# Kernel optimization log

Measured on AMD Instinct MI355X. Metric: run time of the kernel, lower is better.

Reference implementation:

```python
import jax, jax.numpy as jnp
import numpy as np

T, B, H = 1024, 16, 1024
S = 2048


def setup_inputs() -> dict:
    key = jax.random.key(0)
    k1, k2, k3, k4 = jax.random.split(key, 4)
    output = jax.random.normal(k1, (T, B, H), dtype=jnp.float32)
    memory = jax.random.normal(k2, (S, B, H), dtype=jnp.float32)
    attn_mask = jnp.zeros((B, T, S), dtype=jnp.bool_)  # True = masked
    # linear_out: Linear(2H -> H); torch weight layout [out, in]
    W = jax.random.normal(k3, (H, 2 * H), dtype=jnp.float32) * (1.0 / np.sqrt(2 * H))
    b = jax.random.normal(k4, (H,), dtype=jnp.float32) * 0.01
    return {"output": output, "memory": memory, "attn_mask": attn_mask, "W": W, "b": b}


def reference(output, memory, attn_mask, W, b):
    # scores: (B, T, S) = output^T @ memory (unscaled dot product)
    attn = jnp.einsum('tbh,sbh->bts', output, memory)
    attn = jnp.where(attn_mask, -jnp.inf, attn)
    attn = jax.nn.softmax(attn, axis=2)
    # context: (T, B, H)
    context = jnp.einsum('bts,sbh->tbh', attn, memory)
    combined = jnp.concatenate([context, output], axis=2)  # (T, B, 2H)
    out = jnp.tanh(jnp.einsum('tbd,hd->tbh', combined, W) + b)
    return (out, attn)
```

## Files before the change

### kernel.cpp

```cpp
#include <hip/hip_runtime.h>
#include <hip/hip_bf16.h>
#include <math.h>

#define Tn 1024
#define Bn 16
#define Hn 1024
#define Sn 2048

typedef __attribute__((ext_vector_type(8))) short bf16x8;
typedef __attribute__((ext_vector_type(8))) unsigned short u16x8;
typedef __attribute__((ext_vector_type(4))) float f32x4;

__device__ __forceinline__ unsigned short f2bf(float x) {
  unsigned u = __float_as_uint(x);
  u += 0x7fffu + ((u >> 16) & 1u);
  return (unsigned short)(u >> 16);
}
__device__ __forceinline__ float bf2f(unsigned short h) {
  return __uint_as_float(((unsigned)h) << 16);
}

__device__ __forceinline__ void gload16(const void* g, void* l) {
  __builtin_amdgcn_global_load_lds((const __attribute__((address_space(1))) void*)g,
                                   (__attribute__((address_space(3))) void*)l, 16, 0, 0);
}


__global__ __launch_bounds__(256) void k_split_plane(const float* __restrict__ src,
                                                     unsigned short* __restrict__ hiP,
                                                     unsigned short* __restrict__ loP,
                                                     int rows) {
  const int i = blockIdx.x * 256 + threadIdx.x;
  const int h8 = i & (Hn / 8 - 1);
  const int rem = i >> 7;
  const int b = rem & (Bn - 1);
  const int r = rem >> 4;
  const float4 a = *(const float4*)(src + (size_t)i * 8);
  const float4 c = *(const float4*)(src + (size_t)i * 8 + 4);
  const float v[8] = {a.x, a.y, a.z, a.w, c.x, c.y, c.z, c.w};
  u16x8 hv, lv;
#pragma unroll
  for (int j = 0; j < 8; ++j) {
    const unsigned short h = f2bf(v[j]);
    hv[j] = h;
    lv[j] = f2bf(v[j] - bf2f(h));
  }
  const size_t dst = ((size_t)b * rows + r) * Hn + h8 * 8;
  *(u16x8*)(hiP + dst) = hv;
  *(u16x8*)(loP + dst) = lv;
}

__global__ __launch_bounds__(256) void k_cvt8(const float* __restrict__ src,
                                              unsigned short* __restrict__ dst, int n8) {
  const int i = blockIdx.x * 256 + threadIdx.x;
  if (i >= n8) return;
  const float4 a = *(const float4*)(src + (size_t)i * 8);
  const float4 c = *(const float4*)(src + (size_t)i * 8 + 4);
  u16x8 u;
  u[0] = f2bf(a.x); u[1] = f2bf(a.y); u[2] = f2bf(a.z); u[3] = f2bf(a.w);
  u[4] = f2bf(c.x); u[5] = f2bf(c.y); u[6] = f2bf(c.z); u[7] = f2bf(c.w);
  *(u16x8*)(dst + (size_t)i * 8) = u;
}

__global__ __launch_bounds__(256) void k_trH(const unsigned short* __restrict__ memH,
                                             unsigned short* __restrict__ memT) {
  __shared__ unsigned short L[64 * 72];
  const int t = threadIdx.x;
  const int h0 = blockIdx.x * 64, s0 = blockIdx.y * 64, b = blockIdx.z;
#pragma unroll
  for (int p = 0; p < 2; ++p) {
    const int fid = p * 256 + t;
    const int s_l = fid >> 3;
    const int c = fid & 7;
    const u16x8 v = *(const u16x8*)(memH + ((size_t)b * Sn + s0 + s_l) * Hn + h0 + c * 8);
#pragma unroll
    for (int e = 0; e < 8; ++e) L[(c * 8 + e) * 72 + s_l] = v[e];
  }
  __syncthreads();
#pragma unroll
  for (int p = 0; p < 2; ++p) {
    const int cid = p * 256 + t;
    const int h_l = cid >> 3;
    const int c = cid & 7;
    const u16x8 vv = *(const u16x8*)&L[h_l * 72 + c * 8];
    *(u16x8*)(memT + ((size_t)b * Hn + h0 + h_l) * Sn + s0 + c * 8) = vv;
  }
}


__device__ __forceinline__ void stage256x64(const unsigned short* __restrict__ g, size_t ldr,
                                            unsigned short* __restrict__ lds, int tid) {
#pragma unroll
  for (int r = 0; r < 4; ++r) {
    const int row = r * 64 + (tid >> 3);
    const int cb = (tid & 7) * 16;
    const int cs = cb ^ ((row & 4) << 3);
    gload16((const char*)g + (size_t)row * ldr * 2 + cs, (char*)lds + r * 8192 + tid * 16);
  }
}

__device__ __forceinline__ void stage256x32(const unsigned short* __restrict__ g, size_t ldr,
                                            unsigned short* __restrict__ lds, int tid) {
#pragma unroll
  for (int r = 0; r < 2; ++r) {
    const int row = r * 128 + (tid >> 2);
    const int cb = (tid & 3) * 16;
    const int cs = cb ^ ((row & 8) << 2);
    gload16((const char*)g + (size_t)row * ldr * 2 + cs, (char*)lds + r * 8192 + tid * 16);
  }
}


__global__ __launch_bounds__(512, 2) void k_scores(const unsigned short* __restrict__ oH,
                                                   const unsigned short* __restrict__ oL,
                                                   const unsigned short* __restrict__ mH,
                                                   const unsigned short* __restrict__ mL,
                                                   float* __restrict__ attn) {
  __shared__ unsigned short AsH[2][256 * 32], AsL[2][256 * 32];
  __shared__ unsigned short BsH[2][256 * 32], BsL[2][256 * 32];
  const int tid = threadIdx.x, lane = tid & 63, wv = tid >> 6;
  const int wr = wv >> 2, wc = wv & 3;
  const int bs = blockIdx.x * 256, bt = blockIdx.y * 256, b = blockIdx.z;
  const f32x4 fz = {0.f, 0.f, 0.f, 0.f};
  f32x4 acc[8][4];
#pragma unroll
  for (int i = 0; i < 8; ++i)
#pragma unroll
    for (int j = 0; j < 4; ++j) acc[i][j] = fz;

  const unsigned short* AgH = oH + ((size_t)b * Tn + bt) * Hn;
  const unsigned short* AgL = oL + ((size_t)b * Tn + bt) * Hn;
  const unsigned short* BgH = mH + ((size_t)b * Sn + bs) * Hn;
  const unsigned short* BgL = mL + ((size_t)b * Sn + bs) * Hn;
  const int r16 = lane & 15, khB = (lane >> 4) * 16;
  const int NK = Hn / 32;

  stage256x32(AgH, Hn, AsH[0], tid);
  stage256x32(AgL, Hn, AsL[0], tid);
  stage256x32(BgH, Hn, BsH[0], tid);
  stage256x32(BgL, Hn, BsL[0], tid);

  for (int t = 0; t < NK; ++t) {
    const int cur = t & 1;
    if (t + 1 < NK) {
      const int k0 = (t + 1) * 32;
      stage256x32(AgH + k0, Hn, AsH[cur ^ 1], tid);
      stage256x32(AgL + k0, Hn, AsL[cur ^ 1], tid);
      stage256x32(BgH + k0, Hn, BsH[cur ^ 1], tid);
      stage256x32(BgL + k0, Hn, BsL[cur ^ 1], tid);
      asm volatile("s_waitcnt vmcnt(8)" ::: "memory");
    } else {
      asm volatile("s_waitcnt vmcnt(0)" ::: "memory");
    }
    __builtin_amdgcn_s_barrier();

    const char* ABh = (const char*)AsH[cur];
    const char* ABl = (const char*)AsL[cur];
    const char* BBh = (const char*)BsH[cur];
    const char* BBl = (const char*)BsL[cur];
    bf16x8 bh[2][2], bl[2][2];
#pragma unroll
    for (int nq = 0; nq < 2; ++nq)
#pragma unroll
      for (int fj = 0; fj < 2; ++fj) {
        const int rb = wc * 64 + nq * 32 + fj * 16 + r16;
        const int off = rb * 64 + (khB ^ ((rb & 8) << 2));
        bh[nq][fj] = *(const bf16x8*)(BBh + off);
        bl[nq][fj] = *(const bf16x8*)(BBl + off);
      }
#pragma unroll
    for (int mq = 0; mq < 2; ++mq) {
      bf16x8 ah[4], al[4];
#pragma unroll
      for (int fi = 0; fi < 4; ++fi) {
        const int ra = wr * 128 + mq * 64 + fi * 16 + r16;
        const int off = ra * 64 + (khB ^ ((ra & 8) << 2));
        ah[fi] = *(const bf16x8*)(ABh + off);
        al[fi] = *(const bf16x8*)(ABl + off);
      }
      __builtin_amdgcn_s_setprio(1);
#pragma unroll
      for (int nq = 0; nq < 2; ++nq)
#pragma unroll
        for (int fj = 0; fj < 2; ++fj)
#pragma unroll
          for (int fi = 0; fi < 4; ++fi) {
            f32x4& a = acc[mq * 4 + fi][nq * 2 + fj];
            a = __builtin_amdgcn_mfma_f32_16x16x32_bf16(ah[fi], bh[nq][fj], a, 0, 0, 0);
            a = __builtin_amdgcn_mfma_f32_16x16x32_bf16(ah[fi], bl[nq][fj], a, 0, 0, 0);
            a = __builtin_amdgcn_mfma_f32_16x16x32_bf16(al[fi], bh[nq][fj], a, 0, 0, 0);
          }
      __builtin_amdgcn_s_setprio(0);
    }
    __builtin_amdgcn_s_barrier();
  }
  const int rq = (lane >> 4) * 4;
  float* obase = attn + (size_t)b * Tn * Sn;
#pragma unroll
  for (int i = 0; i < 8; ++i) {
    const int m_off = wr * 128 + (i >> 2) * 64 + (i & 3) * 16;
#pragma unroll
    for (int q = 0; q < 4; ++q) {
      const int t = bt + m_off + rq + q;
#pragma unroll
      for (int j = 0; j < 4; ++j) {
        const int s = bs + wc * 64 + (j >> 1) * 32 + (j & 1) * 16 + r16;
        obase[(size_t)t * Sn + s] = acc[i][j][q];
      }
    }
  }
}


__global__ __launch_bounds__(256) void k_softmax(float* __restrict__ attn,
                                                 const unsigned char* __restrict__ mask,
                                                 unsigned short* __restrict__ attnbf) {
  const int row = blockIdx.x;
  float* p = attn + (size_t)row * Sn;
  const unsigned char* mrow = mask + (size_t)row * Sn;
  const int tid = threadIdx.x;
  const int lane = tid & 63;
  const int wv = tid >> 6;
  const float4 a = *(const float4*)(p + tid * 8);
  const float4 c = *(const float4*)(p + tid * 8 + 4);
  const unsigned long long mv = *(const unsigned long long*)(mrow + tid * 8);
  float x[8] = {a.x, a.y, a.z, a.w, c.x, c.y, c.z, c.w};
#pragma unroll
  for (int j = 0; j < 8; ++j)
    if ((mv >> (8 * j)) & 0xffull) x[j] = -INFINITY;
  float mx = x[0];
#pragma unroll
  for (int j = 1; j < 8; ++j) mx = fmaxf(mx, x[j]);
#pragma unroll
  for (int off = 32; off; off >>= 1) mx = fmaxf(mx, __shfl_xor(mx, off, 64));
  __shared__ float redmax[4], redsum[4];
  if (lane == 0) redmax[wv] = mx;
  __syncthreads();
  mx = fmaxf(fmaxf(redmax[0], redmax[1]), fmaxf(redmax[2], redmax[3]));
  float e[8];
  float s = 0.f;
#pragma unroll
  for (int j = 0; j < 8; ++j) {
    e[j] = __expf(x[j] - mx);
    s += e[j];
  }
#pragma unroll
  for (int off = 32; off; off >>= 1) s += __shfl_xor(s, off, 64);
  if (lane == 0) redsum[wv] = s;
  __syncthreads();
  s = redsum[0] + redsum[1] + redsum[2] + redsum[3];
  const float inv = 1.0f / s;
  float o[8];
#pragma unroll
  for (int j = 0; j < 8; ++j) o[j] = e[j] * inv;
  float4 o0 = {o[0], o[1], o[2], o[3]};
  float4 o1 = {o[4], o[5], o[6], o[7]};
  *(float4*)(p + tid * 8) = o0;
  *(float4*)(p + tid * 8 + 4) = o1;
  u16x8 ub;
#pragma unroll
  for (int j = 0; j < 8; ++j) ub[j] = f2bf(o[j]);
  *(u16x8*)(attnbf + (size_t)row * Sn + tid * 8) = ub;
}


__global__ __launch_bounds__(512, 2) void k_context(const unsigned short* __restrict__ attnbf,
                                                    const unsigned short* __restrict__ memT,
                                                    unsigned short* __restrict__ ctxB) {
  __shared__ unsigned short As[2][256 * 64], Bs[2][256 * 64];
  const int tid = threadIdx.x, lane = tid & 63, wv = tid >> 6;
  const int wr = wv >> 2, wc = wv & 3;
  const int bh = blockIdx.x * 256, bt = blockIdx.y * 256, b = blockIdx.z;
  const f32x4 fz = {0.f, 0.f, 0.f, 0.f};
  f32x4 acc[8][4];
#pragma unroll
  for (int i = 0; i < 8; ++i)
#pragma unroll
    for (int j = 0; j < 4; ++j) acc[i][j] = fz;

  const unsigned short* Ag = attnbf + ((size_t)b * Tn + bt) * Sn;
  const unsigned short* Bg = memT + ((size_t)b * Hn + bh) * Sn;
  const int r16 = lane & 15, khB = (lane >> 4) * 16;
  const int NK = Sn / 64;

  stage256x64(Ag, Sn, As[0], tid);
  stage256x64(Bg, Sn, Bs[0], tid);

  for (int t = 0; t < NK; ++t) {
    const int cur = t & 1;
    if (t + 1 < NK) {
      const int k0 = (t + 1) * 64;
      stage256x64(Ag + k0, Sn, As[cur ^ 1], tid);
      stage256x64(Bg + k0, Sn, Bs[cur ^ 1], tid);
      asm volatile("s_waitcnt vmcnt(8)" ::: "memory");
    } else {
      asm volatile("s_waitcnt vmcnt(0)" ::: "memory");
    }
    __builtin_amdgcn_s_barrier();

    const char* Ab = (const char*)As[cur];
    const char* Bb = (const char*)Bs[cur];
    bf16x8 bb[2][2][2];
#pragma unroll
    for (int nq = 0; nq < 2; ++nq)
#pragma unroll
      for (int fj = 0; fj < 2; ++fj) {
        const int rb = wc * 64 + nq * 32 + fj * 16 + r16;
#pragma unroll
        for (int ks = 0; ks < 2; ++ks) {
          const int cb = ks * 64 + khB;
          bb[nq][fj][ks] = *(const bf16x8*)(Bb + rb * 128 + (cb ^ ((rb & 4) << 3)));
        }
      }
#pragma unroll
    for (int mq = 0; mq < 2; ++mq) {
      bf16x8 aa[4][2];
#pragma unroll
      for (int fi = 0; fi < 4; ++fi) {
        const int ra = wr * 128 + mq * 64 + fi * 16 + r16;
#pragma unroll
        for (int ks = 0; ks < 2; ++ks) {
          const int cb = ks * 64 + khB;
          aa[fi][ks] = *(const bf16x8*)(Ab + ra * 128 + (cb ^ ((ra & 4) << 3)));
        }
      }
      __builtin_amdgcn_s_setprio(1);
#pragma unroll
      for (int nq = 0; nq < 2; ++nq)
#pragma unroll
        for (int fj = 0; fj < 2; ++fj)
#pragma unroll
          for (int fi = 0; fi < 4; ++fi)
#pragma unroll
            for (int ks = 0; ks < 2; ++ks) {
              f32x4& a = acc[mq * 4 + fi][nq * 2 + fj];
              a = __builtin_amdgcn_mfma_f32_16x16x32_bf16(aa[fi][ks], bb[nq][fj][ks], a, 0, 0, 0);
            }
      __builtin_amdgcn_s_setprio(0);
    }
    __builtin_amdgcn_s_barrier();
  }
  const int rq = (lane >> 4) * 4;
#pragma unroll
  for (int i = 0; i < 8; ++i) {
    const int m_off = wr * 128 + (i >> 2) * 64 + (i & 3) * 16;
#pragma unroll
    for (int q = 0; q < 4; ++q) {
      const int t = bt + m_off + rq + q;
#pragma unroll
      for (int j = 0; j < 4; ++j) {
        const int h = bh + wc * 64 + (j >> 1) * 32 + (j & 1) * 16 + r16;
        ctxB[((size_t)b * Tn + t) * Hn + h] = f2bf(acc[i][j][q]);
      }
    }
  }
}


__global__ __launch_bounds__(512, 2) void k_final(const unsigned short* __restrict__ ctxB,
                                                  const unsigned short* __restrict__ outpH,
                                                  const unsigned short* __restrict__ Wbf,
                                                  const float* __restrict__ bias,
                                                  float* __restrict__ out) {
  __shared__ unsigned short As[2][256 * 64], Bs[2][256 * 64];
  const int tid = threadIdx.x, lane = tid & 63, wv = tid >> 6;
  const int wr = wv >> 2, wc = wv & 3;
  const int bh = blockIdx.x * 256, bm = blockIdx.y * 256;
  const f32x4 fz = {0.f, 0.f, 0.f, 0.f};
  f32x4 acc[8][4];
#pragma unroll
  for (int i = 0; i < 8; ++i)
#pragma unroll
    for (int j = 0; j < 4; ++j) acc[i][j] = fz;

  const int r16 = lane & 15, khB = (lane >> 4) * 16;
  const int NK = (2 * Hn) / 64;
  auto Asrc = [&](int tt) -> const unsigned short* {
    return (tt < 16) ? (ctxB + (size_t)bm * Hn + tt * 64)
                     : (outpH + (size_t)bm * Hn + (tt - 16) * 64);
  };
  const unsigned short* Bg = Wbf + (size_t)bh * (2 * Hn);

  stage256x64(Asrc(0), Hn, As[0], tid);
  stage256x64(Bg, 2 * Hn, Bs[0], tid);

  for (int t = 0; t < NK; ++t) {
    const int cur = t & 1;
    if (t + 1 < NK) {
      stage256x64(Asrc(t + 1), Hn, As[cur ^ 1], tid);
      stage256x64(Bg + (t + 1) * 64, 2 * Hn, Bs[cur ^ 1], tid);
      asm volatile("s_waitcnt vmcnt(8)" ::: "memory");
    } else {
      asm volatile("s_waitcnt vmcnt(0)" ::: "memory");
    }
    __builtin_amdgcn_s_barrier();

    const char* Ab = (const char*)As[cur];
    const char* Bb = (const char*)Bs[cur];
    bf16x8 bb[2][2][2];
#pragma unroll
    for (int nq = 0; nq < 2; ++nq)
#pragma unroll
      for (int fj = 0; fj < 2; ++fj) {
        const int rb = wc * 64 + nq * 32 + fj * 16 + r16;
#pragma unroll
        for (int ks = 0; ks < 2; ++ks) {
          const int cb = ks * 64 + khB;
          bb[nq][fj][ks] = *(const bf16x8*)(Bb + rb * 128 + (cb ^ ((rb & 4) << 3)));
        }
      }
#pragma unroll
    for (int mq = 0; mq < 2; ++mq) {
      bf16x8 aa[4][2];
#pragma unroll
      for (int fi = 0; fi < 4; ++fi) {
        const int ra = wr * 128 + mq * 64 + fi * 16 + r16;
#pragma unroll
        for (int ks = 0; ks < 2; ++ks) {
          const int cb = ks * 64 + khB;
          aa[fi][ks] = *(const bf16x8*)(Ab + ra * 128 + (cb ^ ((ra & 4) << 3)));
        }
      }
      __builtin_amdgcn_s_setprio(1);
#pragma unroll
      for (int nq = 0; nq < 2; ++nq)
#pragma unroll
        for (int fj = 0; fj < 2; ++fj)
#pragma unroll
          for (int fi = 0; fi < 4; ++fi)
#pragma unroll
            for (int ks = 0; ks < 2; ++ks) {
              f32x4& a = acc[mq * 4 + fi][nq * 2 + fj];
              a = __builtin_amdgcn_mfma_f32_16x16x32_bf16(aa[fi][ks], bb[nq][fj][ks], a, 0, 0, 0);
            }
      __builtin_amdgcn_s_setprio(0);
    }
    __builtin_amdgcn_s_barrier();
  }
  const int rq = (lane >> 4) * 4;
#pragma unroll
  for (int i = 0; i < 8; ++i) {
    const int m_off = wr * 128 + (i >> 2) * 64 + (i & 3) * 16;
#pragma unroll
    for (int q = 0; q < 4; ++q) {
      const int r = bm + m_off + rq + q;
      const int b = r >> 10, t = r & (Tn - 1);
#pragma unroll
      for (int j = 0; j < 4; ++j) {
        const int h = bh + wc * 64 + (j >> 1) * 32 + (j & 1) * 16 + r16;
        out[((size_t)t * Bn + b) * Hn + h] = tanhf(acc[i][j][q] + bias[h]);
      }
    }
  }
}

extern "C" void kernel_launch(void* const* d_in, const int* in_sizes, int n_in,
                              void* d_out, int out_size, void* d_ws, size_t ws_size,
                              hipStream_t stream) {
  const float* outp = (const float*)d_in[0];
  const float* mem = (const float*)d_in[1];
  const unsigned char* mask = (const unsigned char*)d_in[2];
  const float* W = (const float*)d_in[3];
  const float* bias = (const float*)d_in[4];
  float* out = (float*)d_out;
  float* attn = out + (size_t)Tn * Bn * Hn;

  char* w = (char*)d_ws;
  unsigned short* memH  = (unsigned short*)(w);
  unsigned short* memL  = (unsigned short*)(w + ((size_t)64 << 20));
  unsigned short* outpH = (unsigned short*)(w + ((size_t)128 << 20));
  unsigned short* outpL = (unsigned short*)(w + ((size_t)160 << 20));
  unsigned short* Wbf   = (unsigned short*)(w + ((size_t)192 << 20));
  unsigned short* memT   = memL;
  unsigned short* attnbf = memH;
  unsigned short* ctxB   = outpL;

  k_split_plane<<<dim3((Tn * Bn * Hn / 8) / 256), 256, 0, stream>>>(outp, outpH, outpL, Tn);
  k_split_plane<<<dim3((Sn * Bn * Hn / 8) / 256), 256, 0, stream>>>(mem, memH, memL, Sn);
  k_cvt8<<<dim3((Hn * 2 * Hn / 8) / 256), 256, 0, stream>>>(W, Wbf, Hn * 2 * Hn / 8);

  k_scores<<<dim3(Sn / 256, Tn / 256, Bn), 512, 0, stream>>>(outpH, outpL, memH, memL, attn);
  k_trH<<<dim3(Hn / 64, Sn / 64, Bn), 256, 0, stream>>>(memH, memT);
  k_softmax<<<dim3(Bn * Tn), 256, 0, stream>>>(attn, mask, attnbf);
  k_context<<<dim3(Hn / 256, Tn / 256, Bn), 512, 0, stream>>>(attnbf, memT, ctxB);
  k_final<<<dim3(Hn / 256, (Tn * Bn) / 256), 512, 0, stream>>>(ctxB, outpH, Wbf, bias, out);
}
```

Measured before the change: 550.6 us.

## Load A fragments directly to registers and triple-buffer B with interleaved staging

The scores GEMM no longer stages the A (output) tiles through LDS. Each wave now reads its A fragments straight from global memory into registers. B (memory) tiles go into a three-deep LDS ring, with their global-to-LDS loads split into four parts interleaved between the MFMA groups, and the trailing per-iteration barrier is removed. The aim is to cut LDS traffic and footprint, drop one barrier per k-step and overlap B staging with compute. The cost is that the A global loads are issued without prefetch, so their latency may be exposed, and the four waves sharing a row block fetch the same A data redundantly through the caches.

After: 701.7 us. 27.4% more time.

```diff
diff --git a/kernel.cpp b/kernel.cpp
--- a/kernel.cpp
+++ b/kernel.cpp
@@ -99,15 +99,12 @@
   }
 }
 
-__device__ __forceinline__ void stage256x32(const unsigned short* __restrict__ g, size_t ldr,
-                                            unsigned short* __restrict__ lds, int tid) {
-#pragma unroll
-  for (int r = 0; r < 2; ++r) {
-    const int row = r * 128 + (tid >> 2);
-    const int cb = (tid & 3) * 16;
-    const int cs = cb ^ ((row & 8) << 2);
-    gload16((const char*)g + (size_t)row * ldr * 2 + cs, (char*)lds + r * 8192 + tid * 16);
-  }
+__device__ __forceinline__ void stageB32_part(const unsigned short* __restrict__ g,
+                                              unsigned short* __restrict__ lds, int tid, int r) {
+  const int row = r * 128 + (tid >> 2);
+  const int cb = (tid & 3) * 16;
+  const int cs = cb ^ ((row & 8) << 2);
+  gload16((const char*)g + (size_t)row * Hn * 2 + cs, (char*)lds + r * 8192 + tid * 16);
 }
 
 
@@ -116,8 +113,7 @@
                                                    const unsigned short* __restrict__ mH,
                                                    const unsigned short* __restrict__ mL,
                                                    float* __restrict__ attn) {
-  __shared__ unsigned short AsH[2][256 * 32], AsL[2][256 * 32];
-  __shared__ unsigned short BsH[2][256 * 32], BsL[2][256 * 32];
+  __shared__ unsigned short BsH[3][256 * 32], BsL[3][256 * 32];
   const int tid = threadIdx.x, lane = tid & 63, wv = tid >> 6;
   const int wr = wv >> 2, wc = wv & 3;
   const int bs = blockIdx.x * 256, bt = blockIdx.y * 256, b = blockIdx.z;
@@ -128,72 +124,79 @@
 #pragma unroll
     for (int j = 0; j < 4; ++j) acc[i][j] = fz;
 
-  const unsigned short* AgH = oH + ((size_t)b * Tn + bt) * Hn;
-  const unsigned short* AgL = oL + ((size_t)b * Tn + bt) * Hn;
+  const int r16 = lane & 15, khB = (lane >> 4) * 16;
   const unsigned short* BgH = mH + ((size_t)b * Sn + bs) * Hn;
   const unsigned short* BgL = mL + ((size_t)b * Sn + bs) * Hn;
-  const int r16 = lane & 15, khB = (lane >> 4) * 16;
+  const unsigned short* AgH = oH + ((size_t)b * Tn + bt + wr * 128 + r16) * Hn + (lane >> 4) * 8;
+  const unsigned short* AgL = oL + ((size_t)b * Tn + bt + wr * 128 + r16) * Hn + (lane >> 4) * 8;
   const int NK = Hn / 32;
 
-  stage256x32(AgH, Hn, AsH[0], tid);
-  stage256x32(AgL, Hn, AsL[0], tid);
-  stage256x32(BgH, Hn, BsH[0], tid);
-  stage256x32(BgL, Hn, BsL[0], tid);
+  stageB32_part(BgH, BsH[0], tid, 0);
+  stageB32_part(BgH, BsH[0], tid, 1);
+  stageB32_part(BgL, BsL[0], tid, 0);
+  stageB32_part(BgL, BsL[0], tid, 1);
+  stageB32_part(BgH + 32, BsH[1], tid, 0);
+  stageB32_part(BgH + 32, BsH[1], tid, 1);
+  stageB32_part(BgL + 32, BsL[1], tid, 0);
+  stageB32_part(BgL + 32, BsL[1], tid, 1);
 
   for (int t = 0; t < NK; ++t) {
-    const int cur = t & 1;
-    if (t + 1 < NK) {
-      const int k0 = (t + 1) * 32;
-      stage256x32(AgH + k0, Hn, AsH[cur ^ 1], tid);
-      stage256x32(AgL + k0, Hn, AsL[cur ^ 1], tid);
-      stage256x32(BgH + k0, Hn, BsH[cur ^ 1], tid);
-      stage256x32(BgL + k0, Hn, BsL[cur ^ 1], tid);
-      asm volatile("s_waitcnt vmcnt(8)" ::: "memory");
-    } else {
+    if (t + 1 < NK)
+      asm volatile("s_waitcnt vmcnt(4)" ::: "memory");
+    else
       asm volatile("s_waitcnt vmcnt(0)" ::: "memory");
-    }
     __builtin_amdgcn_s_barrier();
 
-    const char* ABh = (const char*)AsH[cur];
-    const char* ABl = (const char*)AsL[cur];
-    const char* BBh = (const char*)BsH[cur];
-    const char* BBl = (const char*)BsL[cur];
+    const int br = t % 3;
+    const int bw = (t + 2) % 3;
+    const bool st = (t + 2) < NK;
+    const int k0 = t * 32;
+
+    bf16x8 ah[2][4], al[2][4];
+#pragma unroll
+    for (int mq = 0; mq < 2; ++mq)
+#pragma unroll
+      for (int fi = 0; fi < 4; ++fi) {
+        const size_t o = (size_t)(mq * 64 + fi * 16) * Hn + k0;
+        ah[mq][fi] = *(const bf16x8*)(AgH + o);
+        al[mq][fi] = *(const bf16x8*)(AgL + o);
+      }
+
+    const char* BH = (const char*)BsH[br];
+    const char* BL = (const char*)BsL[br];
     bf16x8 bh[2][2], bl[2][2];
 #pragma unroll
-    for (int nq = 0; nq < 2; ++nq)
-#pragma unroll
-      for (int fj = 0; fj < 2; ++fj) {
-        const int rb = wc * 64 + nq * 32 + fj * 16 + r16;
-        const int off = rb * 64 + (khB ^ ((rb & 8) << 2));
-        bh[nq][fj] = *(const bf16x8*)(BBh + off);
-        bl[nq][fj] = *(const bf16x8*)(BBl + off);
-      }
-#pragma unroll
-    for (int mq = 0; mq < 2; ++mq) {
-      bf16x8 ah[4], al[4];
-#pragma unroll
-      for (int fi = 0; fi < 4; ++fi) {
-        const int ra = wr * 128 + mq * 64 + fi * 16 + r16;
-        const int off = ra * 64 + (khB ^ ((ra & 8) << 2));
-        ah[fi] = *(const bf16x8*)(ABh + off);
-        al[fi] = *(const bf16x8*)(ABl + off);
+    for (int q = 0; q < 4; ++q) {
+      const int mq = q >> 1, nq = q & 1;
+      if (mq == 0) {
+#pragma unroll
+        for (int fj = 0; fj < 2; ++fj) {
+          const int rb = wc * 64 + nq * 32 + fj * 16 + r16;
+          const int off = rb * 64 + (khB ^ ((rb & 8) << 2));
+          bh[nq][fj] = *(const bf16x8*)(BH + off);
+          bl[nq][fj] = *(const bf16x8*)(BL + off);
+        }
+      }
+      if (st) {
+        if (q == 0) stageB32_part(BgH + (size_t)(k0 + 64), BsH[bw], tid, 0);
+        if (q == 1) stageB32_part(BgH + (size_t)(k0 + 64), BsH[bw], tid, 1);
+        if (q == 2) stageB32_part(BgL + (size_t)(k0 + 64), BsL[bw], tid, 0);
+        if (q == 3) stageB32_part(BgL + (size_t)(k0 + 64), BsL[bw], tid, 1);
       }
       __builtin_amdgcn_s_setprio(1);
 #pragma unroll
-      for (int nq = 0; nq < 2; ++nq)
-#pragma unroll
-        for (int fj = 0; fj < 2; ++fj)
-#pragma unroll
-          for (int fi = 0; fi < 4; ++fi) {
-            f32x4& a = acc[mq * 4 + fi][nq * 2 + fj];
-            a = __builtin_amdgcn_mfma_f32_16x16x32_bf16(ah[fi], bh[nq][fj], a, 0, 0, 0);
-            a = __builtin_amdgcn_mfma_f32_16x16x32_bf16(ah[fi], bl[nq][fj], a, 0, 0, 0);
-            a = __builtin_amdgcn_mfma_f32_16x16x32_bf16(al[fi], bh[nq][fj], a, 0, 0, 0);
-          }
+      for (int fj = 0; fj < 2; ++fj)
+#pragma unroll
+        for (int fi = 0; fi < 4; ++fi) {
+          f32x4& a2 = acc[mq * 4 + fi][nq * 2 + fj];
+          a2 = __builtin_amdgcn_mfma_f32_16x16x32_bf16(ah[mq][fi], bh[nq][fj], a2, 0, 0, 0);
+          a2 = __builtin_amdgcn_mfma_f32_16x16x32_bf16(ah[mq][fi], bl[nq][fj], a2, 0, 0, 0);
+          a2 = __builtin_amdgcn_mfma_f32_16x16x32_bf16(al[mq][fi], bh[nq][fj], a2, 0, 0, 0);
+        }
       __builtin_amdgcn_s_setprio(0);
     }
-    __builtin_amdgcn_s_barrier();
-  }
+  }
+
   const int rq = (lane >> 4) * 4;
   float* obase = attn + (size_t)b * Tn * Sn;
 #pragma unroll
```
